# Optimization experiments

Measured on AMD Instinct MI355X. Metric: run time of the kernel, lower is better.

The kernel has to match this reference:

```python
import jax, jax.numpy as jnp
import numpy as np

B = 1
Z, H, W = 8, 48, 180
C = 384
HEADS = 12
WS = (2, 6, 10)  # window size (z, h, w)
N = WS[0] * WS[1] * WS[2]          # 120 tokens per window
NW = (Z // WS[0]) * (H // WS[1]) * (W // WS[2])  # 576 windows
BIAS_ROWS = (2 * WS[2] - 1) * WS[1] * WS[1] * WS[0] * WS[0]  # 2736


def _position_index(ws):
    w0, w1, w2 = ws
    zi = np.arange(w0); zj = -np.arange(w0) * w0
    hi = np.arange(w1); hj = -np.arange(w1) * w1
    ww = np.arange(w2)
    c1 = np.stack(np.meshgrid(zi, hi, ww, indexing='ij')).reshape(3, -1)
    c2 = np.stack(np.meshgrid(zj, hj, ww, indexing='ij')).reshape(3, -1)
    coords = (c1[:, :, None] - c2[:, None, :]).transpose(1, 2, 0).copy()  # (N, N, 3)
    coords[:, :, 2] += w2 - 1
    coords[:, :, 1] *= 2 * w2 - 1
    coords[:, :, 0] *= (2 * w2 - 1) * w1 * w1
    return jnp.asarray(coords.sum(-1).reshape(-1), dtype=jnp.int32)  # (N*N,)

POS_IDX = _position_index(WS)


def setup_inputs() -> dict:
    key = jax.random.key(0)
    ks = jax.random.split(key, 16)
    s = 0.02
    return {
        'x': jax.random.normal(ks[0], (B, Z * H * W, C), dtype=jnp.float32),
        'wqkv': jax.random.normal(ks[1], (C, 3 * C), dtype=jnp.float32) * s,
        'bqkv': jnp.zeros((3 * C,), dtype=jnp.float32),
        'wproj': jax.random.normal(ks[2], (C, C), dtype=jnp.float32) * s,
        'bproj': jnp.zeros((C,), dtype=jnp.float32),
        'bias_table': jax.random.normal(ks[3], (BIAS_ROWS, NW, HEADS), dtype=jnp.float32) * s,
        'g1': jnp.ones((C,), dtype=jnp.float32),
        'b1': jnp.zeros((C,), dtype=jnp.float32),
        'g2': jnp.ones((C,), dtype=jnp.float32),
        'b2': jnp.zeros((C,), dtype=jnp.float32),
        'wm1': jax.random.normal(ks[4], (C, 4 * C), dtype=jnp.float32) * s,
        'bm1': jnp.zeros((4 * C,), dtype=jnp.float32),
        'wm2': jax.random.normal(ks[5], (4 * C, C), dtype=jnp.float32) * s,
        'bm2': jnp.zeros((C,), dtype=jnp.float32),
    }


def _layernorm(x, g, b, eps=1e-5):
    mu = jnp.mean(x, axis=-1, keepdims=True)
    var = jnp.var(x, axis=-1, keepdims=True)
    return (x - mu) * jax.lax.rsqrt(var + eps) * g + b


def _block(x, wqkv, bqkv, wproj, bproj, bias_table, g1, b1, g2, b2, wm1, bm1, wm2, bm2):
    w0, w1, w2 = WS
    d = C // HEADS
    scale = d ** -0.5
    shortcut = x
    xr = x.reshape(B, Z, H, W, C)
    # window_partition -> (B*nW, N, C)
    xw = xr.reshape(B, Z // w0, w0, H // w1, w1, W // w2, w2, C)
    xw = xw.transpose(0, 1, 3, 5, 2, 4, 6, 7).reshape(-1, N, C)
    # qkv projection, split heads: (3, B*nW, heads, N, d)
    qkv = (xw @ wqkv + bqkv).reshape(-1, N, 3, HEADS, d).transpose(2, 0, 3, 1, 4)
    q, k, v = qkv[0], qkv[1], qkv[2]
    attn = jnp.einsum('whnd,whmd->whnm', q * scale, k)  # (B*nW, heads, N, N)
    # earth-specific bias: gather + reshape to (nW, heads, N, N)
    bias = bias_table[POS_IDX].reshape(N, N, NW, HEADS).transpose(2, 3, 0, 1)
    attn = jax.nn.softmax(attn + bias, axis=-1)
    out = jnp.einsum('whnm,whmd->whnd', attn, v)
    # NOTE: source reshapes (B*nW, heads, N, d) -> (B*nW, N, C) directly (no transpose)
    out = out.reshape(-1, N, C)
    out = out @ wproj + bproj
    # window_reverse -> (B, Z*H*W, C)
    xr = out.reshape(B, Z // w0, H // w1, W // w2, w0, w1, w2, C)
    xr = xr.transpose(0, 1, 4, 2, 5, 3, 6, 7).reshape(B, Z * H * W, C)
    x = shortcut + _layernorm(xr, g1, b1)
    # MLP with post-norm residual
    h = jax.nn.gelu(x @ wm1 + bm1, approximate=False)
    m = h @ wm2 + bm2
    return x + _layernorm(m, g2, b2)


def reference(x, wqkv, bqkv, wproj, bproj, bias_table, g1, b1, g2, b2, wm1, bm1, wm2, bm2):
    return _block(x, wqkv, bqkv, wproj, bproj, bias_table, g1, b1, g2, b2, wm1, bm1, wm2, bm2)
```

## Files before the change

kernel.cpp:

```cpp
#include <hip/hip_runtime.h>
#include <math.h>

#define L_TOK 69120
#define C_DIM 384
#define C3 1152
#define C4 1536
#define N_TOK 120
#define N_HEAD 12
#define BIAS_ROWS 2736
#define WH 6912
#define CHUNK 13824
#define NCHUNK 5

typedef __attribute__((ext_vector_type(8))) short short8;
typedef __attribute__((ext_vector_type(4))) float floatx4;

__device__ __forceinline__ unsigned short f2bf(float f) {
    union { float f; unsigned int u; } c; c.f = f;
    unsigned int u = c.u;
    return (unsigned short)((u + 0x7fffu + ((u >> 16) & 1u)) >> 16);
}
__device__ __forceinline__ float bf2f(unsigned short s) {
    union { unsigned int u; float f; } c; c.u = ((unsigned int)s) << 16;
    return c.f;
}

__device__ __forceinline__ void gl_lds16(const void* g, void* l) {
    __builtin_amdgcn_global_load_lds((const __attribute__((address_space(1))) unsigned int*)g,
                                     (__attribute__((address_space(3))) unsigned int*)l, 16, 0, 0);
}

__device__ __forceinline__ int win_to_global(int m) {
    int w_idx = m / N_TOK;
    int n = m - w_idx * N_TOK;
    int zw = w_idx / 144;
    int rem = w_idx - zw * 144;
    int hw = rem / 18;
    int ww = rem - hw * 18;
    int zl = n / 60;
    int r2 = n - zl * 60;
    int hl = r2 / 10;
    int wl = r2 - hl * 10;
    return ((zw * 2 + zl) * 48 + hw * 6 + hl) * 180 + ww * 10 + wl;
}

__global__ __launch_bounds__(256) void k_wt(const float* __restrict__ W,
                                            unsigned short* __restrict__ WT, int K, int N) {
    __shared__ float tle[32][33];
    int n0 = blockIdx.x << 5, k0 = blockIdx.y << 5;
    for (int i = threadIdx.y; i < 32; i += 8)
        tle[i][threadIdx.x] = W[(size_t)(k0 + i) * N + n0 + threadIdx.x];
    __syncthreads();
    for (int i = threadIdx.y; i < 32; i += 8)
        WT[(size_t)(n0 + i) * K + k0 + threadIdx.x] = f2bf(tle[threadIdx.x][i]);
}

__global__ __launch_bounds__(256) void k_bt(const float* __restrict__ Bsrc,
                                            unsigned short* __restrict__ BTt) {
    __shared__ float tle[32][33];
    int c0 = blockIdx.x << 5;
    int r0 = blockIdx.y << 5;
    for (int i = threadIdx.y; i < 32; i += 8) {
        int r = r0 + i;
        if (r < BIAS_ROWS) tle[i][threadIdx.x] = Bsrc[(size_t)r * WH + c0 + threadIdx.x];
    }
    __syncthreads();
    int rr = r0 + threadIdx.x;
    if (rr < BIAS_ROWS)
        for (int i = threadIdx.y; i < 32; i += 8)
            BTt[(size_t)(c0 + i) * BIAS_ROWS + rr] = f2bf(tle[threadIdx.x][i]);
}

__global__ __launch_bounds__(256) void k_xc(const float* __restrict__ x,
                                            unsigned short* __restrict__ xb) {
    const int m = (blockIdx.x << 2) + (threadIdx.x >> 6);
    const int lane = threadIdx.x & 63;
    const float* src = x + (size_t)win_to_global(m) * C_DIM + lane * 6;
    unsigned short* dst = xb + (size_t)m * C_DIM + lane * 6;
    float2 a = *(const float2*)(src);
    float2 b = *(const float2*)(src + 2);
    float2 c = *(const float2*)(src + 4);
    unsigned int u0 = (unsigned int)f2bf(a.x) | ((unsigned int)f2bf(a.y) << 16);
    unsigned int u1 = (unsigned int)f2bf(b.x) | ((unsigned int)f2bf(b.y) << 16);
    unsigned int u2 = (unsigned int)f2bf(c.x) | ((unsigned int)f2bf(c.y) << 16);
    *(unsigned int*)(dst) = u0;
    *(unsigned int*)(dst + 2) = u1;
    *(unsigned int*)(dst + 4) = u2;
}

template <int K>
__device__ __forceinline__ void mfma_loop(const unsigned short* __restrict__ A,
                                          const unsigned short* __restrict__ BT,
                                          unsigned short* As, unsigned short* Bs,
                                          int m0, int n0, floatx4 acc[4][4]) {
    const int tid = threadIdx.x;
    const int wave = tid >> 6, lane = tid & 63;
    const int wm = (wave >> 1) << 6, wn = (wave & 1) << 6;
    const int lm = lane & 15, lq = lane >> 4;
    const int srow = lane >> 2, scol = (lane & 3) << 3;
    const unsigned short* ags = A + (size_t)(m0 + wave * 32 + srow) * K + scol;
    const unsigned short* bgs = BT + (size_t)(n0 + wave * 32 + srow) * K + scol;
    char* lA = (char*)As + wave * 2048;
    char* lB = (char*)Bs + wave * 2048;
    for (int kk = 0; kk < K; kk += 32) {
        gl_lds16(ags + kk, lA);
        gl_lds16(ags + (size_t)16 * K + kk, lA + 1024);
        gl_lds16(bgs + kk, lB);
        gl_lds16(bgs + (size_t)16 * K + kk, lB + 1024);
        __syncthreads();
        short8 af[4], bq[4];
#pragma unroll
        for (int i = 0; i < 4; ++i) af[i] = *(const short8*)(As + (wm + i * 16 + lm) * 32 + lq * 8);
#pragma unroll
        for (int j = 0; j < 4; ++j) bq[j] = *(const short8*)(Bs + (wn + j * 16 + lm) * 32 + lq * 8);
#pragma unroll
        for (int i = 0; i < 4; ++i)
#pragma unroll
            for (int j = 0; j < 4; ++j)
                acc[i][j] = __builtin_amdgcn_mfma_f32_16x16x32_bf16(af[i], bq[j], acc[i][j], 0, 0, 0);
        __syncthreads();
    }
}

__global__ __launch_bounds__(256) void k_qkv(const unsigned short* __restrict__ xb,
                                             const unsigned short* __restrict__ wqkvT,
                                             const float* __restrict__ bqkv,
                                             unsigned short* __restrict__ q,
                                             unsigned short* __restrict__ kbuf,
                                             unsigned short* __restrict__ vbuf) {
    __shared__ unsigned short As[128 * 32];
    __shared__ unsigned short Bs[128 * 32];
    const int tid = threadIdx.x;
    const int wave = tid >> 6, lane = tid & 63;
    const int wm = (wave >> 1) << 6, wn = (wave & 1) << 6;
    const int lm = lane & 15, lq = lane >> 4;
    const int m0 = blockIdx.y << 7, n0 = blockIdx.x << 7;
    floatx4 acc[4][4];
#pragma unroll
    for (int i = 0; i < 4; ++i)
#pragma unroll
        for (int j = 0; j < 4; ++j) acc[i][j] = (floatx4){0.f, 0.f, 0.f, 0.f};
    mfma_loop<C_DIM>(xb, wqkvT, As, Bs, m0, n0, acc);

    const int sel = n0 / C_DIM;
    unsigned short* dst = (sel == 0) ? q : (sel == 1) ? kbuf : vbuf;
    const float scl = (sel == 0) ? 0.17677669529663687f : 1.0f;
#pragma unroll
    for (int i = 0; i < 4; ++i) {
        int rowb = m0 + wm + i * 16 + lq * 4;
        int wi[4], nn[4];
#pragma unroll
        for (int r = 0; r < 4; ++r) {
            int row = rowb + r;
            wi[r] = row / N_TOK;
            nn[r] = row - wi[r] * N_TOK;
        }
#pragma unroll
        for (int j = 0; j < 4; ++j) {
            int colg = n0 + wn + j * 16 + lm;
            float bias = bqkv[colg];
            int c2 = colg - sel * C_DIM;
            int head = c2 >> 5, dd = c2 & 31;
#pragma unroll
            for (int r = 0; r < 4; ++r) {
                unsigned short val = f2bf((acc[i][j][r] + bias) * scl);
                if (sel == 2)
                    dst[((size_t)(wi[r] * N_HEAD + head) * 32 + dd) * N_TOK + nn[r]] = val;
                else
                    dst[(((size_t)(wi[r] * N_HEAD + head) * N_TOK + nn[r]) << 5) + dd] = val;
            }
        }
    }
}

__global__ __launch_bounds__(256) void k_attn(const unsigned short* __restrict__ q,
                                              const unsigned short* __restrict__ k,
                                              const unsigned short* __restrict__ vt,
                                              const unsigned short* __restrict__ btabT,
                                              unsigned short* __restrict__ ao) {
    const int wh = blockIdx.x;
    const int w = wh / N_HEAD;
    const int h = wh - w * N_HEAD;
    __shared__ float blds[BIAS_ROWS];
    __shared__ __align__(16) unsigned short plds[4][16 * 136];
    const int tid = threadIdx.x;
    const unsigned short* bptr = btabT + (size_t)wh * BIAS_ROWS;
    for (int i = tid; i < BIAS_ROWS; i += 256) blds[i] = bf2f(bptr[i]);
    __syncthreads();

    const int wave = tid >> 6, lane = tid & 63;
    const int lm = lane & 15, lq = lane >> 4;
    const unsigned short* kwh = k + (size_t)wh * N_TOK * 32;
    const unsigned short* qwh = q + (size_t)wh * N_TOK * 32;
    const unsigned short* vwh = vt + (size_t)wh * 32 * N_TOK;
    unsigned short* pl = plds[wave];

    short8 kfr[8];
#pragma unroll
    for (int kt = 0; kt < 8; ++kt)
        kfr[kt] = *(const short8*)(kwh + (size_t)(kt * 16 + lm) * 32 + lq * 8);

    int p0v[8], d2v[8], d3v[8];
#pragma unroll
    for (int kt = 0; kt < 8; ++kt) {
        int k0 = kt * 16 + lq * 4;
        int z2 = (k0 >= 60) ? 1 : 0;
        int k0m = k0 - 60 * z2;
        int h2 = k0m / 10;
        int w2 = k0m - 10 * h2;
        p0v[kt] = z2 * 1368 + h2 * 114 - w2;
        d2v[kt] = (w2 == 8) ? 122 : -2;
        d3v[kt] = (w2 == 8) ? 121 : -3;
    }

    for (int qi = 0; qi < 2; ++qi) {
        const int qt = wave + 4 * qi;
        short8 qfr = *(const short8*)(qwh + (size_t)(qt * 16 + lm) * 32 + lq * 8);
        floatx4 sc[8];
#pragma unroll
        for (int kt = 0; kt < 8; ++kt)
            sc[kt] = __builtin_amdgcn_mfma_f32_16x16x32_bf16(kfr[kt], qfr,
                                                             (floatx4){0.f, 0.f, 0.f, 0.f}, 0, 0, 0);
        int qg = qt * 16 + lm;
        int zl = qg / 60;
        int r2 = qg - zl * 60;
        int hl = r2 / 10;
        int wl = r2 - hl * 10;
        int pbase = zl * 684 + hl * 19 + wl + 9;
        pbase = min(pbase, 797);
#pragma unroll
        for (int kt = 0; kt < 8; ++kt) {
            if (kt == 7 && lq >= 2) {
                sc[kt] = (floatx4){-1e30f, -1e30f, -1e30f, -1e30f};
            } else {
                int base = pbase + p0v[kt];
                sc[kt][0] += blds[base];
                sc[kt][1] += blds[base - 1];
                sc[kt][2] += blds[base + d2v[kt]];
                sc[kt][3] += blds[base + d3v[kt]];
            }
        }
        float mx = -1e30f;
#pragma unroll
        for (int kt = 0; kt < 8; ++kt)
#pragma unroll
            for (int r = 0; r < 4; ++r) mx = fmaxf(mx, sc[kt][r]);
        mx = fmaxf(mx, __shfl_xor(mx, 16, 64));
        mx = fmaxf(mx, __shfl_xor(mx, 32, 64));
        float l = 0.f;
#pragma unroll
        for (int kt = 0; kt < 8; ++kt)
#pragma unroll
            for (int r = 0; r < 4; ++r) {
                float p = __expf(sc[kt][r] - mx);
                sc[kt][r] = p;
                l += p;
            }
        l += __shfl_xor(l, 16, 64);
        l += __shfl_xor(l, 32, 64);
        float inv = 1.f / l;
#pragma unroll
        for (int kt = 0; kt < 8; ++kt) {
            uint2 pk;
            pk.x = (unsigned int)f2bf(sc[kt][0] * inv) | ((unsigned int)f2bf(sc[kt][1] * inv) << 16);
            pk.y = (unsigned int)f2bf(sc[kt][2] * inv) | ((unsigned int)f2bf(sc[kt][3] * inv) << 16);
            *(uint2*)(pl + lm * 136 + kt * 16 + lq * 4) = pk;
        }
        floatx4 oac[2] = {(floatx4){0.f, 0.f, 0.f, 0.f}, (floatx4){0.f, 0.f, 0.f, 0.f}};
#pragma unroll
        for (int ks = 0; ks < 4; ++ks) {
            short8 af = *(const short8*)(pl + lm * 136 + ks * 32 + lq * 8);
#pragma unroll
            for (int ct = 0; ct < 2; ++ct) {
                short8 bf = *(const short8*)(vwh + (size_t)(ct * 16 + lm) * N_TOK + ks * 32 + lq * 8);
                oac[ct] = __builtin_amdgcn_mfma_f32_16x16x32_bf16(af, bf, oac[ct], 0, 0, 0);
            }
        }
#pragma unroll
        for (int r = 0; r < 4; ++r) {
            int qg2 = qt * 16 + lq * 4 + r;
            if (qg2 < N_TOK) {
                int rq = qg2 / 12;
                int rr = h * 10 + rq;
                int cc = (qg2 - rq * 12) * 32;
#pragma unroll
                for (int ct = 0; ct < 2; ++ct)
                    ao[((size_t)w * N_TOK + rr) * C_DIM + cc + ct * 16 + lm] = f2bf(oac[ct][r]);
            }
        }
    }
}

__global__ __launch_bounds__(256) void k_proj(const unsigned short* __restrict__ ao,
                                              const unsigned short* __restrict__ wprojT,
                                              const float* __restrict__ bproj,
                                              float* __restrict__ p) {
    __shared__ unsigned short As[128 * 32];
    __shared__ unsigned short Bs[128 * 32];
    const int tid = threadIdx.x;
    const int wave = tid >> 6, lane = tid & 63;
    const int wm = (wave >> 1) << 6, wn = (wave & 1) << 6;
    const int lm = lane & 15, lq = lane >> 4;
    const int m0 = blockIdx.y << 7, n0 = blockIdx.x << 7;
    floatx4 acc[4][4];
#pragma unroll
    for (int i = 0; i < 4; ++i)
#pragma unroll
        for (int j = 0; j < 4; ++j) acc[i][j] = (floatx4){0.f, 0.f, 0.f, 0.f};
    mfma_loop<C_DIM>(ao, wprojT, As, Bs, m0, n0, acc);
#pragma unroll
    for (int i = 0; i < 4; ++i) {
        int rowb = m0 + wm + i * 16 + lq * 4;
        int gg[4];
#pragma unroll
        for (int r = 0; r < 4; ++r) gg[r] = win_to_global(rowb + r);
#pragma unroll
        for (int j = 0; j < 4; ++j) {
            int colg = n0 + wn + j * 16 + lm;
            float bias = bproj[colg];
#pragma unroll
            for (int r = 0; r < 4; ++r)
                p[(size_t)gg[r] * C_DIM + colg] = acc[i][j][r] + bias;
        }
    }
}

__global__ __launch_bounds__(256) void k_mlp1(const unsigned short* __restrict__ x1b,
                                              const unsigned short* __restrict__ wm1T,
                                              const float* __restrict__ bm1,
                                              unsigned short* __restrict__ hbuf) {
    __shared__ unsigned short As[128 * 32];
    __shared__ unsigned short Bs[128 * 32];
    const int tid = threadIdx.x;
    const int wave = tid >> 6, lane = tid & 63;
    const int wm = (wave >> 1) << 6, wn = (wave & 1) << 6;
    const int lm = lane & 15, lq = lane >> 4;
    const int m0 = blockIdx.y << 7, n0 = blockIdx.x << 7;
    floatx4 acc[4][4];
#pragma unroll
    for (int i = 0; i < 4; ++i)
#pragma unroll
        for (int j = 0; j < 4; ++j) acc[i][j] = (floatx4){0.f, 0.f, 0.f, 0.f};
    mfma_loop<C_DIM>(x1b, wm1T, As, Bs, m0, n0, acc);
#pragma unroll
    for (int i = 0; i < 4; ++i) {
        int rowb = m0 + wm + i * 16 + lq * 4;
#pragma unroll
        for (int j = 0; j < 4; ++j) {
            int colg = n0 + wn + j * 16 + lm;
            float bias = bm1[colg];
#pragma unroll
            for (int r = 0; r < 4; ++r) {
                float vv = acc[i][j][r] + bias;
                float ge = 0.5f * vv * (1.f + erff(vv * 0.70710678118654752f));
                hbuf[(size_t)(rowb + r) * C4 + colg] = f2bf(ge);
            }
        }
    }
}

__global__ __launch_bounds__(256) void k_mlp2(const unsigned short* __restrict__ hbuf,
                                              const unsigned short* __restrict__ wm2T,
                                              const float* __restrict__ bm2,
                                              float* __restrict__ mbuf) {
    __shared__ unsigned short As[128 * 32];
    __shared__ unsigned short Bs[128 * 32];
    const int tid = threadIdx.x;
    const int wave = tid >> 6, lane = tid & 63;
    const int wm = (wave >> 1) << 6, wn = (wave & 1) << 6;
    const int lm = lane & 15, lq = lane >> 4;
    const int m0 = blockIdx.y << 7, n0 = blockIdx.x << 7;
    floatx4 acc[4][4];
#pragma unroll
    for (int i = 0; i < 4; ++i)
#pragma unroll
        for (int j = 0; j < 4; ++j) acc[i][j] = (floatx4){0.f, 0.f, 0.f, 0.f};
    mfma_loop<C4>(hbuf, wm2T, As, Bs, m0, n0, acc);
#pragma unroll
    for (int i = 0; i < 4; ++i) {
        int rowb = m0 + wm + i * 16 + lq * 4;
#pragma unroll
        for (int j = 0; j < 4; ++j) {
            int colg = n0 + wn + j * 16 + lm;
            float bias = bm2[colg];
#pragma unroll
            for (int r = 0; r < 4; ++r)
                mbuf[(size_t)(rowb + r) * C_DIM + colg] = acc[i][j][r] + bias;
        }
    }
}

__global__ __launch_bounds__(128) void k_ln_res(const float* __restrict__ src,
                                                const float* __restrict__ resid,
                                                const float* __restrict__ gamma,
                                                const float* __restrict__ beta,
                                                float* __restrict__ outp,
                                                unsigned short* __restrict__ out_bf) {
    const int row = blockIdx.x;
    const int t = threadIdx.x;
    const float* sr = src + (size_t)row * C_DIM;
    float v0 = sr[t], v1 = sr[t + 128], v2 = sr[t + 256];
    __shared__ float rs[128], rq[128];
    rs[t] = v0 + v1 + v2;
    rq[t] = v0 * v0 + v1 * v1 + v2 * v2;
    __syncthreads();
    for (int off = 64; off > 0; off >>= 1) {
        if (t < off) { rs[t] += rs[t + off]; rq[t] += rq[t + off]; }
        __syncthreads();
    }
    float mu = rs[0] * (1.f / 384.f);
    float var = rq[0] * (1.f / 384.f) - mu * mu;
    float rinv = rsqrtf(var + 1e-5f);
    const float* rr = resid + (size_t)row * C_DIM;
    float* orow = outp + (size_t)row * C_DIM;
    float y0 = rr[t]       + (v0 - mu) * rinv * gamma[t]       + beta[t];
    float y1 = rr[t + 128] + (v1 - mu) * rinv * gamma[t + 128] + beta[t + 128];
    float y2 = rr[t + 256] + (v2 - mu) * rinv * gamma[t + 256] + beta[t + 256];
    orow[t] = y0; orow[t + 128] = y1; orow[t + 256] = y2;
    if (out_bf) {
        unsigned short* ob = out_bf + (size_t)row * C_DIM;
        ob[t] = f2bf(y0); ob[t + 128] = f2bf(y1); ob[t + 256] = f2bf(y2);
    }
}

extern "C" void kernel_launch(void* const* d_in, const int* in_sizes, int n_in,
                              void* d_out, int out_size, void* d_ws, size_t ws_size,
                              hipStream_t stream) {
    const float* x     = (const float*)d_in[0];
    const float* wqkv  = (const float*)d_in[1];
    const float* bqkv  = (const float*)d_in[2];
    const float* wproj = (const float*)d_in[3];
    const float* bproj = (const float*)d_in[4];
    const float* btab  = (const float*)d_in[5];
    const float* g1    = (const float*)d_in[6];
    const float* b1    = (const float*)d_in[7];
    const float* g2    = (const float*)d_in[8];
    const float* b2    = (const float*)d_in[9];
    const float* wm1   = (const float*)d_in[10];
    const float* bm1   = (const float*)d_in[11];
    const float* wm2   = (const float*)d_in[12];
    const float* bm2   = (const float*)d_in[13];
    float* outp = (float*)d_out;

    const size_t LC = (size_t)L_TOK * C_DIM;
    if (ws_size < 8 * LC) return;
    char* ws = (char*)d_ws;
    const size_t QB = LC * 2;
    unsigned short* qb  = (unsigned short*)ws;
    unsigned short* kb  = (unsigned short*)(ws + QB);
    unsigned short* vb  = (unsigned short*)(ws + 2 * QB);
    unsigned short* btT = (unsigned short*)(ws + 3 * QB);
    unsigned short* hbuf = (unsigned short*)(ws + 3 * QB);
    size_t wof = 3 * QB + (size_t)CHUNK * C4 * 2;
    unsigned short* wqkvT = (unsigned short*)(ws + wof);
    unsigned short* wprojT = wqkvT + (size_t)C3 * C_DIM;
    unsigned short* wm1T   = wprojT + (size_t)C_DIM * C_DIM;
    unsigned short* wm2T   = wm1T + (size_t)C_DIM * C4;
    unsigned short* aob = qb;
    float* proj = (float*)(ws + QB);
    float* x1   = proj;
    unsigned short* x1b = qb;
    unsigned short* xbuf = (unsigned short*)d_out;

    dim3 tb(32, 8);
    k_wt<<<dim3(C3 / 32, C_DIM / 32), tb, 0, stream>>>(wqkv, wqkvT, C_DIM, C3);
    k_wt<<<dim3(C_DIM / 32, C_DIM / 32), tb, 0, stream>>>(wproj, wprojT, C_DIM, C_DIM);
    k_wt<<<dim3(C4 / 32, C_DIM / 32), tb, 0, stream>>>(wm1, wm1T, C_DIM, C4);
    k_wt<<<dim3(C_DIM / 32, C4 / 32), tb, 0, stream>>>(wm2, wm2T, C4, C_DIM);
    k_bt<<<dim3(WH / 32, (BIAS_ROWS + 31) / 32), tb, 0, stream>>>(btab, btT);

    k_xc<<<dim3(L_TOK / 4), dim3(256), 0, stream>>>(x, xbuf);
    k_qkv<<<dim3(C3 / 128, L_TOK / 128), dim3(256), 0, stream>>>(xbuf, wqkvT, bqkv, qb, kb, vb);
    k_attn<<<dim3(WH), dim3(256), 0, stream>>>(qb, kb, vb, btT, aob);
    k_proj<<<dim3(C_DIM / 128, L_TOK / 128), dim3(256), 0, stream>>>(aob, wprojT, bproj, proj);
    k_ln_res<<<dim3(L_TOK), dim3(128), 0, stream>>>(proj, x, g1, b1, x1, x1b);
    for (int c = 0; c < NCHUNK; ++c) {
        size_t r0 = (size_t)c * CHUNK;
        float* mbuf = outp + r0 * C_DIM;
        k_mlp1<<<dim3(C4 / 128, CHUNK / 128), dim3(256), 0, stream>>>(x1b + r0 * C_DIM, wm1T, bm1, hbuf);
        k_mlp2<<<dim3(C_DIM / 128, CHUNK / 128), dim3(256), 0, stream>>>(hbuf, wm2T, bm2, mbuf);
        k_ln_res<<<dim3(CHUNK), dim3(128), 0, stream>>>(mbuf, x1 + r0 * C_DIM, g2, b2, mbuf, (unsigned short*)nullptr);
    }
    (void)in_sizes; (void)n_in; (void)out_size;
}
```

Baseline: 1.113 ms.

## Stage GEMM epilogues through LDS for vectorized stores, add XCD swizzle

The weight transpose for wqkv and wm1 now permutes output columns so that each lane's four MFMA accumulator columns are contiguous. The qkv and mlp1 epilogues can then pack bf16 results and stage them through a padded LDS tile, writing 16-byte coalesced global stores instead of scattered 2-byte ones. The V path transposes within LDS to keep its token-major layout. GEMM blocks are also remapped with an XCD-aware swizzle to improve L2 locality, and the input conversion kernel uses wider 16-byte loads and stores. The cost is extra LDS use and a barrier in each epilogue.

```diff
diff --git a/kernel.cpp b/kernel.cpp
--- a/kernel.cpp
+++ b/kernel.cpp
@@ -28,6 +28,15 @@
 __device__ __forceinline__ void gl_lds16(const void* g, void* l) {
     __builtin_amdgcn_global_load_lds((const __attribute__((address_space(1))) unsigned int*)g,
                                      (__attribute__((address_space(3))) unsigned int*)l, 16, 0, 0);
+}
+
+__device__ __forceinline__ void xcd_swz(int gx, int nwg, int* bx, int* by) {
+    int orig = blockIdx.y * gx + blockIdx.x;
+    int q8 = nwg >> 3, r8 = nwg & 7;
+    int xcd = orig & 7, lin = orig >> 3;
+    int sw = (xcd < r8 ? xcd * (q8 + 1) : r8 * (q8 + 1) + (xcd - r8) * q8) + lin;
+    *bx = sw % gx;
+    *by = sw / gx;
 }
 
 __device__ __forceinline__ int win_to_global(int m) {
@@ -45,11 +54,14 @@
 }
 
 __global__ __launch_bounds__(256) void k_wt(const float* __restrict__ W,
-                                            unsigned short* __restrict__ WT, int K, int N) {
+                                            unsigned short* __restrict__ WT, int K, int N, int perm) {
     __shared__ float tle[32][33];
     int n0 = blockIdx.x << 5, k0 = blockIdx.y << 5;
-    for (int i = threadIdx.y; i < 32; i += 8)
-        tle[i][threadIdx.x] = W[(size_t)(k0 + i) * N + n0 + threadIdx.x];
+    for (int i = threadIdx.y; i < 32; i += 8) {
+        int n = n0 + threadIdx.x;
+        int src = perm ? ((n & ~63) | ((n & 15) << 2) | ((n >> 4) & 3)) : n;
+        tle[i][threadIdx.x] = W[(size_t)(k0 + i) * N + src];
+    }
     __syncthreads();
     for (int i = threadIdx.y; i < 32; i += 8)
         WT[(size_t)(n0 + i) * K + k0 + threadIdx.x] = f2bf(tle[threadIdx.x][i]);
@@ -73,19 +85,18 @@
 
 __global__ __launch_bounds__(256) void k_xc(const float* __restrict__ x,
                                             unsigned short* __restrict__ xb) {
-    const int m = (blockIdx.x << 2) + (threadIdx.x >> 6);
-    const int lane = threadIdx.x & 63;
-    const float* src = x + (size_t)win_to_global(m) * C_DIM + lane * 6;
-    unsigned short* dst = xb + (size_t)m * C_DIM + lane * 6;
-    float2 a = *(const float2*)(src);
-    float2 b = *(const float2*)(src + 2);
-    float2 c = *(const float2*)(src + 4);
-    unsigned int u0 = (unsigned int)f2bf(a.x) | ((unsigned int)f2bf(a.y) << 16);
-    unsigned int u1 = (unsigned int)f2bf(b.x) | ((unsigned int)f2bf(b.y) << 16);
-    unsigned int u2 = (unsigned int)f2bf(c.x) | ((unsigned int)f2bf(c.y) << 16);
-    *(unsigned int*)(dst) = u0;
-    *(unsigned int*)(dst + 2) = u1;
-    *(unsigned int*)(dst + 4) = u2;
+    int gid = blockIdx.x * 256 + threadIdx.x;
+    int m = gid / 48;
+    int seg = gid - m * 48;
+    const float* src = x + (size_t)win_to_global(m) * C_DIM + seg * 8;
+    float4 a = *(const float4*)(src);
+    float4 b = *(const float4*)(src + 4);
+    uint4 o;
+    o.x = (unsigned int)f2bf(a.x) | ((unsigned int)f2bf(a.y) << 16);
+    o.y = (unsigned int)f2bf(a.z) | ((unsigned int)f2bf(a.w) << 16);
+    o.z = (unsigned int)f2bf(b.x) | ((unsigned int)f2bf(b.y) << 16);
+    o.w = (unsigned int)f2bf(b.z) | ((unsigned int)f2bf(b.w) << 16);
+    *(uint4*)(xb + (size_t)m * C_DIM + seg * 8) = o;
 }
 
 template <int K>
@@ -128,13 +139,17 @@
                                              unsigned short* __restrict__ q,
                                              unsigned short* __restrict__ kbuf,
                                              unsigned short* __restrict__ vbuf) {
-    __shared__ unsigned short As[128 * 32];
-    __shared__ unsigned short Bs[128 * 32];
+    __shared__ __align__(16) unsigned short smem[128 * 136];
+    unsigned short* As = smem;
+    unsigned short* Bs = smem + 128 * 32;
     const int tid = threadIdx.x;
+    int bx, by;
+    xcd_swz(9, 9 * (L_TOK / 128), &bx, &by);
+    const int m0 = by << 7, n0 = bx << 7;
     const int wave = tid >> 6, lane = tid & 63;
     const int wm = (wave >> 1) << 6, wn = (wave & 1) << 6;
     const int lm = lane & 15, lq = lane >> 4;
-    const int m0 = blockIdx.y << 7, n0 = blockIdx.x << 7;
+
     floatx4 acc[4][4];
 #pragma unroll
     for (int i = 0; i < 4; ++i)
@@ -142,33 +157,59 @@
         for (int j = 0; j < 4; ++j) acc[i][j] = (floatx4){0.f, 0.f, 0.f, 0.f};
     mfma_loop<C_DIM>(xb, wqkvT, As, Bs, m0, n0, acc);
 
-    const int sel = n0 / C_DIM;
+    const int sel = bx / 3;
     unsigned short* dst = (sel == 0) ? q : (sel == 1) ? kbuf : vbuf;
     const float scl = (sel == 0) ? 0.17677669529663687f : 1.0f;
-#pragma unroll
-    for (int i = 0; i < 4; ++i) {
-        int rowb = m0 + wm + i * 16 + lq * 4;
-        int wi[4], nn[4];
-#pragma unroll
-        for (int r = 0; r < 4; ++r) {
-            int row = rowb + r;
-            wi[r] = row / N_TOK;
-            nn[r] = row - wi[r] * N_TOK;
-        }
-#pragma unroll
-        for (int j = 0; j < 4; ++j) {
-            int colg = n0 + wn + j * 16 + lm;
-            float bias = bqkv[colg];
-            int c2 = colg - sel * C_DIM;
+    float4 b4 = *(const float4*)(bqkv + n0 + wn + 4 * lm);
+
+    if (sel < 2) {
+#pragma unroll
+        for (int i = 0; i < 4; ++i)
+#pragma unroll
+            for (int r = 0; r < 4; ++r) {
+                uint2 pk;
+                pk.x = (unsigned int)f2bf((acc[i][0][r] + b4.x) * scl) |
+                       ((unsigned int)f2bf((acc[i][1][r] + b4.y) * scl) << 16);
+                pk.y = (unsigned int)f2bf((acc[i][2][r] + b4.z) * scl) |
+                       ((unsigned int)f2bf((acc[i][3][r] + b4.w) * scl) << 16);
+                *(uint2*)(smem + (wm + i * 16 + lq * 4 + r) * 136 + wn + 4 * lm) = pk;
+            }
+        __syncthreads();
+#pragma unroll
+        for (int it = 0; it < 8; ++it) {
+            int s = it * 256 + tid;
+            int row = s >> 4, cs = (s & 15) << 3;
+            uint4 vv = *(const uint4*)(smem + row * 136 + cs);
+            int m = m0 + row;
+            int wi = m / N_TOK, nn = m - wi * N_TOK;
+            int c2 = n0 + cs - sel * C_DIM;
             int head = c2 >> 5, dd = c2 & 31;
-#pragma unroll
-            for (int r = 0; r < 4; ++r) {
-                unsigned short val = f2bf((acc[i][j][r] + bias) * scl);
-                if (sel == 2)
-                    dst[((size_t)(wi[r] * N_HEAD + head) * 32 + dd) * N_TOK + nn[r]] = val;
-                else
-                    dst[(((size_t)(wi[r] * N_HEAD + head) * N_TOK + nn[r]) << 5) + dd] = val;
+            *(uint4*)(dst + (((size_t)(wi * N_HEAD + head) * N_TOK + nn) << 5) + dd) = vv;
+        }
+    } else {
+#pragma unroll
+        for (int i = 0; i < 4; ++i)
+#pragma unroll
+            for (int j = 0; j < 4; ++j) {
+                float bj = (j == 0) ? b4.x : (j == 1) ? b4.y : (j == 2) ? b4.z : b4.w;
+                uint2 pk;
+                pk.x = (unsigned int)f2bf(acc[i][j][0] + bj) |
+                       ((unsigned int)f2bf(acc[i][j][1] + bj) << 16);
+                pk.y = (unsigned int)f2bf(acc[i][j][2] + bj) |
+                       ((unsigned int)f2bf(acc[i][j][3] + bj) << 16);
+                *(uint2*)(smem + (wn + 4 * lm + j) * 136 + wm + i * 16 + lq * 4) = pk;
             }
+        __syncthreads();
+#pragma unroll
+        for (int it = 0; it < 8; ++it) {
+            int s = it * 256 + tid;
+            int c = s >> 4, mo = (s & 15) << 3;
+            uint4 vv = *(const uint4*)(smem + c * 136 + mo);
+            int m = m0 + mo;
+            int wi = m / N_TOK, nn = m - wi * N_TOK;
+            int c2 = n0 + c - 2 * C_DIM;
+            int head = c2 >> 5, dd = c2 & 31;
+            *(uint4*)(dst + ((size_t)(wi * N_HEAD + head) * 32 + dd) * N_TOK + nn) = vv;
         }
     }
 }
@@ -301,7 +342,9 @@
     const int wave = tid >> 6, lane = tid & 63;
     const int wm = (wave >> 1) << 6, wn = (wave & 1) << 6;
     const int lm = lane & 15, lq = lane >> 4;
-    const int m0 = blockIdx.y << 7, n0 = blockIdx.x << 7;
+    int bx, by;
+    xcd_swz(3, 3 * (L_TOK / 128), &bx, &by);
+    const int m0 = by << 7, n0 = bx << 7;
     floatx4 acc[4][4];
 #pragma unroll
     for (int i = 0; i < 4; ++i)
@@ -329,33 +372,48 @@
                                               const unsigned short* __restrict__ wm1T,
                                               const float* __restrict__ bm1,
                                               unsigned short* __restrict__ hbuf) {
-    __shared__ unsigned short As[128 * 32];
-    __shared__ unsigned short Bs[128 * 32];
+    __shared__ __align__(16) unsigned short smem[128 * 136];
+    unsigned short* As = smem;
+    unsigned short* Bs = smem + 128 * 32;
     const int tid = threadIdx.x;
     const int wave = tid >> 6, lane = tid & 63;
     const int wm = (wave >> 1) << 6, wn = (wave & 1) << 6;
     const int lm = lane & 15, lq = lane >> 4;
-    const int m0 = blockIdx.y << 7, n0 = blockIdx.x << 7;
+    int bx, by;
+    xcd_swz(12, 12 * (CHUNK / 128), &bx, &by);
+    const int m0 = by << 7, n0 = bx << 7;
     floatx4 acc[4][4];
 #pragma unroll
     for (int i = 0; i < 4; ++i)
 #pragma unroll
         for (int j = 0; j < 4; ++j) acc[i][j] = (floatx4){0.f, 0.f, 0.f, 0.f};
     mfma_loop<C_DIM>(x1b, wm1T, As, Bs, m0, n0, acc);
-#pragma unroll
-    for (int i = 0; i < 4; ++i) {
-        int rowb = m0 + wm + i * 16 + lq * 4;
-#pragma unroll
-        for (int j = 0; j < 4; ++j) {
-            int colg = n0 + wn + j * 16 + lm;
-            float bias = bm1[colg];
-#pragma unroll
-            for (int r = 0; r < 4; ++r) {
-                float vv = acc[i][j][r] + bias;
-                float ge = 0.5f * vv * (1.f + erff(vv * 0.70710678118654752f));
-                hbuf[(size_t)(rowb + r) * C4 + colg] = f2bf(ge);
-            }
-        }
+
+    float4 b4 = *(const float4*)(bm1 + n0 + wn + 4 * lm);
+#pragma unroll
+    for (int i = 0; i < 4; ++i)
+#pragma unroll
+        for (int r = 0; r < 4; ++r) {
+            float v0 = acc[i][0][r] + b4.x;
+            float v1 = acc[i][1][r] + b4.y;
+            float v2 = acc[i][2][r] + b4.z;
+            float v3 = acc[i][3][r] + b4.w;
+            v0 = 0.5f * v0 * (1.f + erff(v0 * 0.70710678118654752f));
+            v1 = 0.5f * v1 * (1.f + erff(v1 * 0.70710678118654752f));
+            v2 = 0.5f * v2 * (1.f + erff(v2 * 0.70710678118654752f));
+            v3 = 0.5f * v3 * (1.f + erff(v3 * 0.70710678118654752f));
+            uint2 pk;
+            pk.x = (unsigned int)f2bf(v0) | ((unsigned int)f2bf(v1) << 16);
+            pk.y = (unsigned int)f2bf(v2) | ((unsigned int)f2bf(v3) << 16);
+            *(uint2*)(smem + (wm + i * 16 + lq * 4 + r) * 136 + wn + 4 * lm) = pk;
+        }
+    __syncthreads();
+#pragma unroll
+    for (int it = 0; it < 8; ++it) {
+        int s = it * 256 + tid;
+        int row = s >> 4, cs = (s & 15) << 3;
+        uint4 vv = *(const uint4*)(smem + row * 136 + cs);
+        *(uint4*)(hbuf + (size_t)(m0 + row) * C4 + n0 + cs) = vv;
     }
 }
 
@@ -369,7 +427,9 @@
     const int wave = tid >> 6, lane = tid & 63;
     const int wm = (wave >> 1) << 6, wn = (wave & 1) << 6;
     const int lm = lane & 15, lq = lane >> 4;
-    const int m0 = blockIdx.y << 7, n0 = blockIdx.x << 7;
+    int bx, by;
+    xcd_swz(3, 3 * (CHUNK / 128), &bx, &by);
+    const int m0 = by << 7, n0 = bx << 7;
     floatx4 acc[4][4];
 #pragma unroll
     for (int i = 0; i < 4; ++i)
@@ -463,13 +523,13 @@
     unsigned short* xbuf = (unsigned short*)d_out;
 
     dim3 tb(32, 8);
-    k_wt<<<dim3(C3 / 32, C_DIM / 32), tb, 0, stream>>>(wqkv, wqkvT, C_DIM, C3);
-    k_wt<<<dim3(C_DIM / 32, C_DIM / 32), tb, 0, stream>>>(wproj, wprojT, C_DIM, C_DIM);
-    k_wt<<<dim3(C4 / 32, C_DIM / 32), tb, 0, stream>>>(wm1, wm1T, C_DIM, C4);
-    k_wt<<<dim3(C_DIM / 32, C4 / 32), tb, 0, stream>>>(wm2, wm2T, C4, C_DIM);
+    k_wt<<<dim3(C3 / 32, C_DIM / 32), tb, 0, stream>>>(wqkv, wqkvT, C_DIM, C3, 1);
+    k_wt<<<dim3(C_DIM / 32, C_DIM / 32), tb, 0, stream>>>(wproj, wprojT, C_DIM, C_DIM, 0);
+    k_wt<<<dim3(C4 / 32, C_DIM / 32), tb, 0, stream>>>(wm1, wm1T, C_DIM, C4, 1);
+    k_wt<<<dim3(C_DIM / 32, C4 / 32), tb, 0, stream>>>(wm2, wm2T, C4, C_DIM, 0);
     k_bt<<<dim3(WH / 32, (BIAS_ROWS + 31) / 32), tb, 0, stream>>>(btab, btT);
 
-    k_xc<<<dim3(L_TOK / 4), dim3(256), 0, stream>>>(x, xbuf);
+    k_xc<<<dim3(L_TOK * 48 / 256), dim3(256), 0, stream>>>(x, xbuf);
     k_qkv<<<dim3(C3 / 128, L_TOK / 128), dim3(256), 0, stream>>>(xbuf, wqkvT, bqkv, qb, kb, vb);
     k_attn<<<dim3(WH), dim3(256), 0, stream>>>(qb, kb, vb, btT, aob);
     k_proj<<<dim3(C_DIM / 128, L_TOK / 128), dim3(256), 0, stream>>>(aob, wprojT, bproj, proj);
```

Result: faster. 1.089 ms (-2.1%).
